# Performance work log

Hardware: AMD Instinct MI355X
Metric: run time of the kernel (lower is better)

Reference implementation:

```python
import jax, jax.numpy as jnp
import numpy as np

B, T, C, H = 4, 2048, 1024, 16
D = C // H  # head dim = 64


def _layernorm(x, g, b, eps=1e-5):
    mu = jnp.mean(x, axis=-1, keepdims=True)
    var = jnp.var(x, axis=-1, keepdims=True)
    return (x - mu) * jax.lax.rsqrt(var + eps) * g + b


def setup_inputs() -> dict:
    key = jax.random.key(0)
    ks = jax.random.split(key, 8)
    s = 0.02
    return {
        "x": jax.random.normal(ks[0], (B, T, C), dtype=jnp.float32),
        "ln1_g": jnp.ones((C,), jnp.float32),
        "ln1_b": jnp.zeros((C,), jnp.float32),
        "W_qkv": jax.random.normal(ks[1], (C, 3 * C), dtype=jnp.float32) * s,
        "b_qkv": jnp.zeros((3 * C,), jnp.float32),
        "W_o": jax.random.normal(ks[2], (C, C), dtype=jnp.float32) * s,
        "b_o": jnp.zeros((C,), jnp.float32),
        "ln2_g": jnp.ones((C,), jnp.float32),
        "ln2_b": jnp.zeros((C,), jnp.float32),
        "W_fc": jax.random.normal(ks[3], (C, 4 * C), dtype=jnp.float32) * s,
        "b_fc": jnp.zeros((4 * C,), jnp.float32),
        "W_pr": jax.random.normal(ks[4], (4 * C, C), dtype=jnp.float32) * s,
        "b_pr": jnp.zeros((C,), jnp.float32),
    }


def reference(x, ln1_g, ln1_b, W_qkv, b_qkv, W_o, b_o, ln2_g, ln2_b, W_fc, b_fc, W_pr, b_pr):
    # --- attention sub-block ---
    h = _layernorm(x, ln1_g, ln1_b)
    qkv = h @ W_qkv + b_qkv                       # [B,T,3C]
    q, k, v = jnp.split(qkv, 3, axis=-1)
    q = q.reshape(B, T, H, D).transpose(0, 2, 1, 3)  # [B,H,T,D]
    k = k.reshape(B, T, H, D).transpose(0, 2, 1, 3)
    v = v.reshape(B, T, H, D).transpose(0, 2, 1, 3)
    att = jnp.einsum("bhqd,bhkd->bhqk", q, k) * (1.0 / jnp.sqrt(jnp.float32(D)))
    causal = jnp.tril(jnp.ones((T, T), dtype=bool))
    att = jnp.where(causal, att, jnp.float32(-jnp.inf))
    att = jax.nn.softmax(att, axis=-1)
    y = jnp.einsum("bhqk,bhkd->bhqd", att, v)     # [B,H,T,D]
    y = y.transpose(0, 2, 1, 3).reshape(B, T, C)
    y = y @ W_o + b_o
    x = x + y
    # --- FFN sub-block ---
    h2 = _layernorm(x, ln2_g, ln2_b)
    f = jax.nn.gelu(h2 @ W_fc + b_fc, approximate=False)  # nn.GELU default = exact
    f = f @ W_pr + b_pr
    return x + f
```

## Files before the change

### kernel.cpp

```cpp
#include <hip/hip_runtime.h>
#include <math.h>
#include <stdint.h>

#define Bz 4
#define Tz 2048
#define Cz 1024
#define Hz 16
#define Dz 64
#define MTOK (Bz*Tz)

typedef __attribute__((ext_vector_type(8))) short short8;
typedef __attribute__((ext_vector_type(4))) short short4v;
typedef __attribute__((ext_vector_type(4))) float f32x4;

typedef unsigned int u32_g __attribute__((address_space(1)));
typedef unsigned int u32_l __attribute__((address_space(3)));

__device__ __forceinline__ unsigned short f2bf(float f) {
    unsigned int u = __float_as_uint(f);
    u += 0x7fffu + ((u >> 16) & 1u);
    return (unsigned short)(u >> 16);
}
__device__ __forceinline__ float bf2f(unsigned short h) {
    return __uint_as_float((unsigned int)h << 16);
}

__device__ __forceinline__ void async_cp16(const unsigned short* g, unsigned short* l) {
    __builtin_amdgcn_global_load_lds((const u32_g*)g, (u32_l*)l, 16, 0, 0);
}

#define BARX() asm volatile("s_barrier" ::: "memory")
#define VMCM(n) asm volatile("s_waitcnt vmcnt(" #n ")" ::: "memory")
#define LGKMC(n) do { asm volatile("s_waitcnt lgkmcnt(" #n ")" ::: "memory"); \
                      __builtin_amdgcn_sched_barrier(0); } while (0)

__global__ void transpose_wf(const float* __restrict__ W, unsigned short* __restrict__ Bf,
                             int K, int N) {
    const int nf = blockIdx.x;
    const int k0 = blockIdx.y * 128;
    const int tid = threadIdx.x;
    const int ktl = tid >> 6, lane = tid & 63;
    const int col = nf * 16 + (lane & 15);
    const int kk = k0 + ktl * 32 + (lane >> 4) * 8;
    const int KT = K >> 5;
    short8 o;
    #pragma unroll
    for (int j = 0; j < 8; j++)
        o[j] = (short)f2bf(W[(size_t)(kk + j) * N + col]);
    *(short8*)&Bf[(((size_t)nf * KT + (k0 >> 5) + ktl) * 64 + lane) * 8] = o;
}

__global__ void transpose_v(const unsigned short* __restrict__ in, unsigned short* __restrict__ out) {
    __shared__ unsigned short tile[64][68];
    const int bh = blockIdx.x;
    const int t0 = blockIdx.y * 64;
    const int tid = threadIdx.x;
    const int r4 = tid >> 4;
    const int c4 = tid & 15;
    #pragma unroll
    for (int p = 0; p < 4; p++) {
        const int r = p * 16 + r4;
        *(short4v*)&tile[r][c4 * 4] =
            *(const short4v*)&in[((size_t)bh * Tz + t0 + r) * Dz + c4 * 4];
    }
    __syncthreads();
    #pragma unroll
    for (int p = 0; p < 4; p++) {
        const int d = p * 16 + r4;
        short4v o;
        #pragma unroll
        for (int j = 0; j < 4; j++) o[j] = tile[c4 * 4 + j][d];
        *(short4v*)&out[((size_t)bh * Dz + d) * Tz + t0 + c4 * 4] = o;
    }
}

__global__ void ln_kernel(const float* __restrict__ x, const float* __restrict__ g,
                          const float* __restrict__ bb, unsigned short* __restrict__ out) {
    int tok = blockIdx.x, tid = threadIdx.x;
    const float4 v = ((const float4*)(x + (size_t)tok * Cz))[tid];
    float s = v.x + v.y + v.z + v.w;
    float sq = v.x * v.x + v.y * v.y + v.z * v.z + v.w * v.w;
    #pragma unroll
    for (int m = 1; m < 64; m <<= 1) { s += __shfl_xor(s, m); sq += __shfl_xor(sq, m); }
    __shared__ float red[8];
    int lane = tid & 63, wid = tid >> 6;
    if (!lane) { red[wid] = s; red[4 + wid] = sq; }
    __syncthreads();
    s = red[0] + red[1] + red[2] + red[3];
    sq = red[4] + red[5] + red[6] + red[7];
    float mu = s * (1.0f / Cz);
    float var = sq * (1.0f / Cz) - mu * mu;
    float rs = rsqrtf(var + 1e-5f);
    float4 gv = ((const float4*)g)[tid];
    float4 bv = ((const float4*)bb)[tid];
    short4v o;
    o[0] = f2bf((v.x - mu) * rs * gv.x + bv.x);
    o[1] = f2bf((v.y - mu) * rs * gv.y + bv.y);
    o[2] = f2bf((v.z - mu) * rs * gv.z + bv.z);
    o[3] = f2bf((v.w - mu) * rs * gv.w + bv.w);
    *(short4v*)(out + (size_t)tok * Cz + tid * 4) = o;
}

#define MODE_QKV 0
#define MODE_RESID 1
#define MODE_GELU 2

template <int MODE>
__launch_bounds__(256)
__global__ void gemm_rp(const unsigned short* __restrict__ A, const unsigned short* __restrict__ Bf,
                        int K, int N, const float* __restrict__ bias,
                        float* __restrict__ outf, unsigned short* __restrict__ outb,
                        const float* __restrict__ resid,
                        unsigned short* __restrict__ qo, unsigned short* __restrict__ ko,
                        unsigned short* __restrict__ vo) {
    __shared__ __align__(16) unsigned short LDS[4 * 2048];
    const int tid = threadIdx.x;
    const int lane = tid & 63;
    const int gn = tid >> 6;
    const int quad = lane >> 4, l15 = lane & 15;
    const int id = blockIdx.x;
    const int rr = id >> 3;
    const int m0 = ((id & 7) * 16 + (rr & 15)) * 64;
    const int n0 = (rr >> 4) * 256;
    const int NT = K >> 5;
    const int KT = K >> 5;

    const int lseg = (tid & 3) ^ ((tid >> 3) & 3);
    const int srow = tid >> 2;
    const unsigned short* Ag0 = A + (size_t)(m0 + srow) * K + lseg * 8;

    const unsigned ldsA = (unsigned)(uintptr_t)(u32_l*)LDS;
    unsigned offAb[4];
    #pragma unroll
    for (int mi = 0; mi < 4; mi++) {
        const int ra = mi * 16 + l15;
        offAb[mi] = (unsigned)(ra * 64 + ((quad ^ ((ra >> 1) & 3)) << 4));
    }

    const int nfg = (n0 >> 4) + gn * 4;
    const unsigned short* Bp[4];
    #pragma unroll
    for (int ni = 0; ni < 4; ni++)
        Bp[ni] = Bf + ((size_t)(nfg + ni) * KT) * 512 + lane * 8;

    f32x4 acc[4][4] = {};
    short8 afP[4], afQ[4], bfP[4], bfQ[4];

#define GLBa(bfX) do { _Pragma("unroll") for (int ni = 0; ni < 4; ni++) { \
    asm volatile("global_load_dwordx4 %0, %1, off" \
        : "=&v"(bfX[ni]) : "v"((unsigned long long)(uintptr_t)Bp[ni]) : "memory"); \
    Bp[ni] += 512; } } while (0)
#define STG(tt) async_cp16(Ag0 + (size_t)(tt) * 32, LDS + (((unsigned)(tt)) & 3u) * 2048 + tid * 8)
#define RDSa(afX, tt) do { \
    const unsigned sb_ = ldsA + (((unsigned)(tt)) & 3u) * 4096u; \
    _Pragma("unroll") for (int mi = 0; mi < 4; mi++) \
        asm volatile("ds_read_b128 %0, %1" : "=&v"(afX[mi]) : "v"(sb_ + offAb[mi])); } while (0)
#define MMS(afX, bfX) do { \
    __builtin_amdgcn_s_setprio(1); \
    _Pragma("unroll") for (int mi = 0; mi < 4; mi++) \
        _Pragma("unroll") for (int ni = 0; ni < 4; ni++) \
            acc[mi][ni] = __builtin_amdgcn_mfma_f32_16x16x32_bf16(afX[mi], bfX[ni], acc[mi][ni], 0, 0, 0); \
    __builtin_amdgcn_s_setprio(0); } while (0)

    STG(0); STG(1); GLBa(bfP); GLBa(bfQ); STG(2);
    VMCM(5);
    BARX();
    RDSa(afP, 0);

    for (int t = 0; t < NT; t += 2) {
        if (t + 3 < NT) STG(t + 3);
        RDSa(afQ, t + 1);
        LGKMC(4);
        MMS(afP, bfP);
        if (t + 2 < NT) GLBa(bfP);
        if (t + 3 < NT) { VMCM(5); } else { VMCM(0); }
        BARX();
        if (t + 4 < NT) STG(t + 4);
        if (t + 2 < NT) { RDSa(afP, t + 2); LGKMC(4); } else { LGKMC(0); }
        MMS(afQ, bfQ);
        if (t + 3 < NT) GLBa(bfQ);
        if (t + 4 < NT) { VMCM(5); } else { VMCM(0); }
        BARX();
    }
#undef GLBa
#undef STG
#undef RDSa
#undef MMS

    float bv[4];
    #pragma unroll
    for (int ni = 0; ni < 4; ni++) bv[ni] = bias[n0 + gn * 64 + ni * 16 + l15];

    if constexpr (MODE == MODE_QKV) {
        const int colb = n0 + gn * 64;
        const int which = colb >> 10;
        const int hh = (colb & 1023) >> 6;
        unsigned short* dst = (which == 0) ? qo : (which == 1) ? ko : vo;
        #pragma unroll
        for (int mi = 0; mi < 4; mi++) {
            #pragma unroll
            for (int r = 0; r < 4; r++) {
                const int row = m0 + mi * 16 + quad * 4 + r;
                const int b_ = row >> 11, tt = row & 2047;
                unsigned short* rp = dst + ((size_t)(b_ * Hz + hh) * Tz + tt) * Dz;
                #pragma unroll
                for (int ni = 0; ni < 4; ni++)
                    rp[ni * 16 + l15] = f2bf(acc[mi][ni][r] + bv[ni]);
            }
        }
    } else if constexpr (MODE == MODE_RESID) {
        #pragma unroll
        for (int mi = 0; mi < 4; mi++) {
            #pragma unroll
            for (int r = 0; r < 4; r++) {
                const int row = m0 + mi * 16 + quad * 4 + r;
                float* rp = outf + (size_t)row * N + n0 + gn * 64;
                const float* rr_ = resid + (size_t)row * N + n0 + gn * 64;
                #pragma unroll
                for (int ni = 0; ni < 4; ni++) {
                    const int c = ni * 16 + l15;
                    rp[c] = acc[mi][ni][r] + bv[ni] + rr_[c];
                }
            }
        }
    } else {
        #pragma unroll
        for (int mi = 0; mi < 4; mi++) {
            #pragma unroll
            for (int r = 0; r < 4; r++) {
                const int row = m0 + mi * 16 + quad * 4 + r;
                unsigned short* rp = outb + (size_t)row * N + n0 + gn * 64;
                #pragma unroll
                for (int ni = 0; ni < 4; ni++) {
                    float val = acc[mi][ni][r] + bv[ni];
                    float c = val * (1.0f + 0.044715f * val * val);
                    float e = __expf(1.5957691216057308f * c);
                    rp[ni * 16 + l15] = f2bf(val * e / (1.0f + e));
                }
            }
        }
    }
}

#define ATT_SC 0.18033688011112042f
__launch_bounds__(256)
__global__ void attn_kernel(const unsigned short* __restrict__ qb, const unsigned short* __restrict__ kb,
                            const unsigned short* __restrict__ vt, unsigned short* __restrict__ y) {
    __shared__ __align__(16) unsigned short Klds[64 * 64];
    __shared__ __align__(16) unsigned short Vtl[64 * 64];
    __shared__ __align__(16) unsigned short Plds[4][16 * 72];
    const int tid = threadIdx.x;
    const int lane = tid & 63, wid = tid >> 6;
    const int quad = lane >> 4, l15 = lane & 15;
    const int bh = blockIdx.x & 63;
    const int qt = 15 - (int)(blockIdx.x >> 6);
    const size_t baseT = (size_t)bh * Tz;
    const size_t vbase = (size_t)bh * Dz;
    const int qb0 = qt * 128;

    short8 qf[2][2];
    {
        const unsigned short* q0p = qb + (baseT + qb0 + wid * 16 + l15) * Dz + quad * 8;
        qf[0][0] = *(const short8*)q0p;
        qf[0][1] = *(const short8*)(q0p + 32);
        const unsigned short* q1p = q0p + (size_t)64 * Dz;
        qf[1][0] = *(const short8*)q1p;
        qf[1][1] = *(const short8*)(q1p + 32);
    }

    f32x4 o[2][4] = {};
    float lsum[2][4] = {{0.f,0.f,0.f,0.f},{0.f,0.f,0.f,0.f}};

    const int srow = lane >> 3;
    const int swz = ((lane & 7) ^ srow) * 8;
    const unsigned short* kg0 = kb + (baseT + wid * 8 + srow) * Dz + swz;
    const unsigned short* kg1 = kg0 + (size_t)32 * Dz;
    const unsigned short* vg0 = vt + (vbase + wid * 8 + srow) * Tz + swz;
    const unsigned short* vg1 = vg0 + (size_t)32 * Tz;
    unsigned short* kl0 = &Klds[wid * 512 + lane * 8];
    unsigned short* kl1 = kl0 + 2048;
    unsigned short* vl0 = &Vtl[wid * 512 + lane * 8];
    unsigned short* vl1 = vl0 + 2048;

    const int nchunk = 2 * qt + 2;

    for (int ci = 0; ci < nchunk; ci++) {
        const int k0 = ci * 64;
        async_cp16(kg0 + (size_t)k0 * Dz, kl0);
        async_cp16(kg1 + (size_t)k0 * Dz, kl1);
        async_cp16(vg0 + k0, vl0);
        async_cp16(vg1 + k0, vl1);
        __syncthreads();

        #pragma unroll
        for (int t = 0; t < 2; t++) {
            if (t == 0 && ci == nchunk - 1) continue;
            const bool diag = (ci == nchunk - 2 + t);

            f32x4 s[4];
            #pragma unroll
            for (int c = 0; c < 4; c++) {
                const int rk = c * 16 + l15;
                short8 kf0 = *(const short8*)&Klds[rk * 64 + ((quad ^ (rk & 7)) * 8)];
                short8 kf1 = *(const short8*)&Klds[rk * 64 + (((quad + 4) ^ (rk & 7)) * 8)];
                f32x4 z = {};
                z = __builtin_amdgcn_mfma_f32_16x16x32_bf16(qf[t][0], kf0, z, 0, 0, 0);
                s[c] = __builtin_amdgcn_mfma_f32_16x16x32_bf16(qf[t][1], kf1, z, 0, 0, 0);
            }
            const int qr = qb0 + t * 64 + wid * 16 + quad * 4;
            #pragma unroll
            for (int c = 0; c < 4; c++)
                #pragma unroll
                for (int r = 0; r < 4; r++) {
                    float p = exp2f(s[c][r] * ATT_SC);
                    if (diag) {
                        int key = k0 + c * 16 + l15;
                        p = (key <= qr + r) ? p : 0.f;
                    }
                    s[c][r] = p;
                    lsum[t][r] += p;
                }
            unsigned short* P = Plds[wid];
            #pragma unroll
            for (int c = 0; c < 4; c++)
                #pragma unroll
                for (int r = 0; r < 4; r++)
                    P[(quad * 4 + r) * 72 + c * 16 + l15] = f2bf(s[c][r]);
            short8 pf0 = *(const short8*)&P[l15 * 72 + quad * 8];
            short8 pf1 = *(const short8*)&P[l15 * 72 + 32 + quad * 8];
            #pragma unroll
            for (int nc = 0; nc < 4; nc++) {
                const int rv = nc * 16 + l15;
                short8 vf0 = *(const short8*)&Vtl[rv * 64 + ((quad ^ (rv & 7)) * 8)];
                short8 vf1 = *(const short8*)&Vtl[rv * 64 + (((quad + 4) ^ (rv & 7)) * 8)];
                o[t][nc] = __builtin_amdgcn_mfma_f32_16x16x32_bf16(pf0, vf0, o[t][nc], 0, 0, 0);
                o[t][nc] = __builtin_amdgcn_mfma_f32_16x16x32_bf16(pf1, vf1, o[t][nc], 0, 0, 0);
            }
        }
        __syncthreads();
    }

    const int b_ = bh >> 4, hh = bh & 15;
    #pragma unroll
    for (int t = 0; t < 2; t++)
        #pragma unroll
        for (int r = 0; r < 4; r++) {
            float ls = lsum[t][r];
            #pragma unroll
            for (int m = 1; m < 16; m <<= 1) ls += __shfl_xor(ls, m);
            float inv = 1.0f / ls;
            size_t tok = (size_t)qb0 + t * 64 + wid * 16 + quad * 4 + r;
            unsigned short* yr = y + ((size_t)b_ * Tz + tok) * Cz + hh * Dz;
            #pragma unroll
            for (int nc = 0; nc < 4; nc++)
                yr[nc * 16 + l15] = f2bf(o[t][nc][r] * inv);
        }
}

extern "C" void kernel_launch(void* const* d_in, const int* in_sizes, int n_in,
                              void* d_out, int out_size, void* d_ws, size_t ws_size,
                              hipStream_t stream) {
    const float* x    = (const float*)d_in[0];
    const float* ln1g = (const float*)d_in[1];
    const float* ln1b = (const float*)d_in[2];
    const float* Wqkv = (const float*)d_in[3];
    const float* bqkv = (const float*)d_in[4];
    const float* Wo   = (const float*)d_in[5];
    const float* bo   = (const float*)d_in[6];
    const float* ln2g = (const float*)d_in[7];
    const float* ln2b = (const float*)d_in[8];
    const float* Wfc  = (const float*)d_in[9];
    const float* bfc  = (const float*)d_in[10];
    const float* Wpr  = (const float*)d_in[11];
    const float* bpr  = (const float*)d_in[12];
    float* out = (float*)d_out;

    char* ws = (char*)d_ws;
    size_t off = 0;
    auto alloc = [&](size_t bytes) { void* p = ws + off; off += (bytes + 255) & ~(size_t)255; return p; };
    unsigned short* wqkv_t = (unsigned short*)alloc((size_t)3072 * 1024 * 2);
    unsigned short* wo_t   = (unsigned short*)alloc((size_t)1024 * 1024 * 2);
    unsigned short* wfc_t  = (unsigned short*)alloc((size_t)4096 * 1024 * 2);
    unsigned short* wpr_t  = (unsigned short*)alloc((size_t)1024 * 4096 * 2);
    unsigned short* h1     = (unsigned short*)alloc((size_t)MTOK * Cz * 2);
    unsigned short* qbuf   = (unsigned short*)alloc((size_t)MTOK * Cz * 2);
    unsigned short* kbuf   = (unsigned short*)alloc((size_t)MTOK * Cz * 2);
    unsigned short* vbuf   = (unsigned short*)alloc((size_t)MTOK * Cz * 2);
    unsigned short* ybuf   = (unsigned short*)alloc((size_t)MTOK * Cz * 2);
    float*          x1     = (float*)alloc((size_t)MTOK * Cz * 4);
    unsigned short* h2     = (unsigned short*)alloc((size_t)MTOK * Cz * 2);
    unsigned short* fbuf   = (unsigned short*)alloc((size_t)MTOK * 4096 * 2);
    unsigned short* vtmp   = fbuf;

    transpose_wf<<<dim3(3072 / 16, 1024 / 128), 256, 0, stream>>>(Wqkv, wqkv_t, 1024, 3072);
    transpose_wf<<<dim3(1024 / 16, 1024 / 128), 256, 0, stream>>>(Wo, wo_t, 1024, 1024);
    transpose_wf<<<dim3(4096 / 16, 1024 / 128), 256, 0, stream>>>(Wfc, wfc_t, 1024, 4096);
    transpose_wf<<<dim3(1024 / 16, 4096 / 128), 256, 0, stream>>>(Wpr, wpr_t, 4096, 1024);

    ln_kernel<<<MTOK, 256, 0, stream>>>(x, ln1g, ln1b, h1);
    gemm_rp<MODE_QKV><<<1536, 256, 0, stream>>>(h1, wqkv_t, 1024, 3072, bqkv,
                                                nullptr, nullptr, nullptr, qbuf, kbuf, vtmp);
    transpose_v<<<dim3(64, 32), 256, 0, stream>>>(vtmp, vbuf);
    attn_kernel<<<1024, 256, 0, stream>>>(qbuf, kbuf, vbuf, ybuf);
    gemm_rp<MODE_RESID><<<512, 256, 0, stream>>>(ybuf, wo_t, 1024, 1024, bo,
                                                 x1, nullptr, x, nullptr, nullptr, nullptr);
    ln_kernel<<<MTOK, 256, 0, stream>>>(x1, ln2g, ln2b, h2);
    gemm_rp<MODE_GELU><<<2048, 256, 0, stream>>>(h2, wfc_t, 1024, 4096, bfc,
                                                 nullptr, fbuf, nullptr, nullptr, nullptr, nullptr);
    gemm_rp<MODE_RESID><<<512, 256, 0, stream>>>(fbuf, wpr_t, 4096, 1024, bpr,
                                                 out, nullptr, x1, nullptr, nullptr, nullptr);
}
```

Baseline: 499.8 us.

## Double-buffer attention K/V tiles and fold softmax scale into Q projection

The attention kernel now keeps two LDS buffers for K and V and prefetches the next chunk asynchronously while the current one is computed. This replaces the old load-then-sync pattern and its two barriers per chunk with a single wait and barrier. The softmax scale is applied to Q in the QKV GEMM epilogue, removing a multiply per score, and P is packed to bf16 with a paired conversion instruction. Q is rounded to bf16 after scaling, which changes numerics slightly, and doubling the K/V LDS footprint may reduce occupancy.

```diff
diff --git a/kernel.cpp b/kernel.cpp
--- a/kernel.cpp
+++ b/kernel.cpp
@@ -8,6 +8,7 @@
 #define Hz 16
 #define Dz 64
 #define MTOK (Bz*Tz)
+#define ATT_SC 0.18033688011112042f
 
 typedef __attribute__((ext_vector_type(8))) short short8;
 typedef __attribute__((ext_vector_type(4))) short short4v;
@@ -196,6 +197,7 @@
         const int which = colb >> 10;
         const int hh = (colb & 1023) >> 6;
         unsigned short* dst = (which == 0) ? qo : (which == 1) ? ko : vo;
+        const float qsc = (which == 0) ? ATT_SC : 1.0f;
         #pragma unroll
         for (int mi = 0; mi < 4; mi++) {
             #pragma unroll
@@ -205,7 +207,7 @@
                 unsigned short* rp = dst + ((size_t)(b_ * Hz + hh) * Tz + tt) * Dz;
                 #pragma unroll
                 for (int ni = 0; ni < 4; ni++)
-                    rp[ni * 16 + l15] = f2bf(acc[mi][ni][r] + bv[ni]);
+                    rp[ni * 16 + l15] = f2bf((acc[mi][ni][r] + bv[ni]) * qsc);
             }
         }
     } else if constexpr (MODE == MODE_RESID) {
@@ -242,12 +244,11 @@
     }
 }
 
-#define ATT_SC 0.18033688011112042f
 __launch_bounds__(256)
 __global__ void attn_kernel(const unsigned short* __restrict__ qb, const unsigned short* __restrict__ kb,
                             const unsigned short* __restrict__ vt, unsigned short* __restrict__ y) {
-    __shared__ __align__(16) unsigned short Klds[64 * 64];
-    __shared__ __align__(16) unsigned short Vtl[64 * 64];
+    __shared__ __align__(16) unsigned short Klds[2][64 * 64];
+    __shared__ __align__(16) unsigned short Vtl[2][64 * 64];
     __shared__ __align__(16) unsigned short Plds[4][16 * 72];
     const int tid = threadIdx.x;
     const int lane = tid & 63, wid = tid >> 6;
@@ -258,6 +259,22 @@
     const size_t vbase = (size_t)bh * Dz;
     const int qb0 = qt * 128;
 
+    const int srow = lane >> 3;
+    const int swz = ((lane & 7) ^ srow) * 8;
+    const unsigned short* kg0 = kb + (baseT + wid * 8 + srow) * Dz + swz;
+    const unsigned short* kg1 = kg0 + (size_t)32 * Dz;
+    const unsigned short* vg0 = vt + (vbase + wid * 8 + srow) * Tz + swz;
+    const unsigned short* vg1 = vg0 + (size_t)32 * Tz;
+    const int lofs = wid * 512 + lane * 8;
+
+#define ASTG(ci_) do { const int s_ = (ci_) & 1; const int kk_ = (ci_) * 64; \
+    async_cp16(kg0 + (size_t)kk_ * Dz, &Klds[s_][lofs]); \
+    async_cp16(kg1 + (size_t)kk_ * Dz, &Klds[s_][2048 + lofs]); \
+    async_cp16(vg0 + kk_, &Vtl[s_][lofs]); \
+    async_cp16(vg1 + kk_, &Vtl[s_][2048 + lofs]); } while (0)
+
+    ASTG(0);
+
     short8 qf[2][2];
     {
         const unsigned short* q0p = qb + (baseT + qb0 + wid * 16 + l15) * Dz + quad * 8;
@@ -271,26 +288,14 @@
     f32x4 o[2][4] = {};
     float lsum[2][4] = {{0.f,0.f,0.f,0.f},{0.f,0.f,0.f,0.f}};
 
-    const int srow = lane >> 3;
-    const int swz = ((lane & 7) ^ srow) * 8;
-    const unsigned short* kg0 = kb + (baseT + wid * 8 + srow) * Dz + swz;
-    const unsigned short* kg1 = kg0 + (size_t)32 * Dz;
-    const unsigned short* vg0 = vt + (vbase + wid * 8 + srow) * Tz + swz;
-    const unsigned short* vg1 = vg0 + (size_t)32 * Tz;
-    unsigned short* kl0 = &Klds[wid * 512 + lane * 8];
-    unsigned short* kl1 = kl0 + 2048;
-    unsigned short* vl0 = &Vtl[wid * 512 + lane * 8];
-    unsigned short* vl1 = vl0 + 2048;
-
     const int nchunk = 2 * qt + 2;
 
     for (int ci = 0; ci < nchunk; ci++) {
+        VMCM(0);
+        BARX();
+        if (ci + 1 < nchunk) ASTG(ci + 1);
+        const int sl = ci & 1;
         const int k0 = ci * 64;
-        async_cp16(kg0 + (size_t)k0 * Dz, kl0);
-        async_cp16(kg1 + (size_t)k0 * Dz, kl1);
-        async_cp16(vg0 + k0, vl0);
-        async_cp16(vg1 + k0, vl1);
-        __syncthreads();
 
         #pragma unroll
         for (int t = 0; t < 2; t++) {
@@ -301,8 +306,8 @@
             #pragma unroll
             for (int c = 0; c < 4; c++) {
                 const int rk = c * 16 + l15;
-                short8 kf0 = *(const short8*)&Klds[rk * 64 + ((quad ^ (rk & 7)) * 8)];
-                short8 kf1 = *(const short8*)&Klds[rk * 64 + (((quad + 4) ^ (rk & 7)) * 8)];
+                short8 kf0 = *(const short8*)&Klds[sl][rk * 64 + ((quad ^ (rk & 7)) * 8)];
+                short8 kf1 = *(const short8*)&Klds[sl][rk * 64 + (((quad + 4) ^ (rk & 7)) * 8)];
                 f32x4 z = {};
                 z = __builtin_amdgcn_mfma_f32_16x16x32_bf16(qf[t][0], kf0, z, 0, 0, 0);
                 s[c] = __builtin_amdgcn_mfma_f32_16x16x32_bf16(qf[t][1], kf1, z, 0, 0, 0);
@@ -312,7 +317,7 @@
             for (int c = 0; c < 4; c++)
                 #pragma unroll
                 for (int r = 0; r < 4; r++) {
-                    float p = exp2f(s[c][r] * ATT_SC);
+                    float p = exp2f(s[c][r]);
                     if (diag) {
                         int key = k0 + c * 16 + l15;
                         p = (key <= qr + r) ? p : 0.f;
@@ -322,23 +327,29 @@
                 }
             unsigned short* P = Plds[wid];
             #pragma unroll
-            for (int c = 0; c < 4; c++)
+            for (int c = 0; c < 4; c++) {
                 #pragma unroll
-                for (int r = 0; r < 4; r++)
-                    P[(quad * 4 + r) * 72 + c * 16 + l15] = f2bf(s[c][r]);
+                for (int rp2 = 0; rp2 < 2; rp2++) {
+                    unsigned pk;
+                    asm("v_cvt_pk_bf16_f32 %0, %1, %2"
+                        : "=v"(pk) : "v"(s[c][2 * rp2]), "v"(s[c][2 * rp2 + 1]));
+                    P[(quad * 4 + 2 * rp2) * 72 + c * 16 + l15] = (unsigned short)pk;
+                    P[(quad * 4 + 2 * rp2 + 1) * 72 + c * 16 + l15] = (unsigned short)(pk >> 16);
+                }
+            }
             short8 pf0 = *(const short8*)&P[l15 * 72 + quad * 8];
             short8 pf1 = *(const short8*)&P[l15 * 72 + 32 + quad * 8];
             #pragma unroll
             for (int nc = 0; nc < 4; nc++) {
                 const int rv = nc * 16 + l15;
-                short8 vf0 = *(const short8*)&Vtl[rv * 64 + ((quad ^ (rv & 7)) * 8)];
-                short8 vf1 = *(const short8*)&Vtl[rv * 64 + (((quad + 4) ^ (rv & 7)) * 8)];
+                short8 vf0 = *(const short8*)&Vtl[sl][rv * 64 + ((quad ^ (rv & 7)) * 8)];
+                short8 vf1 = *(const short8*)&Vtl[sl][rv * 64 + (((quad + 4) ^ (rv & 7)) * 8)];
                 o[t][nc] = __builtin_amdgcn_mfma_f32_16x16x32_bf16(pf0, vf0, o[t][nc], 0, 0, 0);
                 o[t][nc] = __builtin_amdgcn_mfma_f32_16x16x32_bf16(pf1, vf1, o[t][nc], 0, 0, 0);
             }
         }
-        __syncthreads();
-    }
+    }
+#undef ASTG
 
     const int b_ = bh >> 4, hh = bh & 15;
     #pragma unroll
```

After: 504.1 us. No clear change (+0.8%).
